# Performance work log

Hardware: AMD Instinct MI355X
Metric: run time of the kernel (lower is better)

The kernel has to match this reference:

```python
import jax, jax.numpy as jnp
import numpy as np

NUM_LAYERS = 2


def _lstm_scan(x, w_ih, w_hh):
    """x: [S,B,I]; w_ih: [4H,I]; w_hh: [4H,H]. Returns per-step (hs, cs): [S,B,H]."""
    S, B, _ = x.shape
    H = w_hh.shape[1]
    xg = jnp.einsum('sbi,gi->sbg', x, w_ih)  # precompute input contributions [S,B,4H]

    def step(carry, xg_t):
        h, c = carry
        gates = xg_t + h @ w_hh.T
        i, f, g, o = jnp.split(gates, 4, axis=-1)  # torch LSTM gate order
        i = jax.nn.sigmoid(i)
        f = jax.nn.sigmoid(f)
        g = jnp.tanh(g)
        o = jax.nn.sigmoid(o)
        c = f * c + i * g
        h = o * jnp.tanh(c)
        return (h, c), (h, c)

    init = (jnp.zeros((B, H), x.dtype), jnp.zeros((B, H), x.dtype))
    _, (hs, cs) = jax.lax.scan(step, init, xg)
    return hs, cs


def _stacked(x, w_ih, w_hh, reverse):
    """Stacked unidirectional LSTM. w_ih/w_hh: [L,4H,*].
    Returns (out [S,B,H], h_last [L,B,H], c_last [L,B,H]) matching stackedRNN
    semantics: for reverse, the returned 'last' hidden is the per-step state at
    original time index S-1 (first step processed in the reverse loop)."""
    h_last, c_last = [], []
    cur = x
    for layer in range(w_ih.shape[0]):
        xin = jnp.flip(cur, axis=0) if reverse else cur
        hs, cs = _lstm_scan(xin, w_ih[layer], w_hh[layer])
        if reverse:
            hs = jnp.flip(hs, axis=0)
            cs = jnp.flip(cs, axis=0)
        cur = hs
        h_last.append(hs[-1])  # faithful to torch code's layer[-1] indexing
        c_last.append(cs[-1])
    return cur, jnp.stack(h_last, 0), jnp.stack(c_last, 0)


def setup_inputs() -> dict:
    key = jax.random.key(0)
    ks = jax.random.split(key, 5)
    S, B, I, H, L = 256, 32, 1024, 1024, NUM_LAYERS
    stdev = 1.0 / np.sqrt(H)
    u = lambda k, shape: jax.random.uniform(k, shape, jnp.float32, -stdev, stdev)
    return {
        'x': jax.random.normal(ks[0], (S, B, I), jnp.float32),
        'w_ih_fwd': u(ks[1], (L, 4 * H, I)),
        'w_hh_fwd': u(ks[2], (L, 4 * H, H)),
        'w_ih_bwd': u(ks[3], (L, 4 * H, I)),
        'w_hh_bwd': u(ks[4], (L, 4 * H, H)),
    }


def reference(x, w_ih_fwd, w_hh_fwd, w_ih_bwd, w_hh_bwd):
    out_f, h_f, c_f = _stacked(x, w_ih_fwd, w_hh_fwd, reverse=False)
    out_b, h_b, c_b = _stacked(x, w_ih_bwd, w_hh_bwd, reverse=True)
    output = jnp.concatenate([out_f, out_b], axis=-1)      # [S,B,2H]
    h_all = jnp.concatenate([h_f, h_b], axis=-1)            # [L,B,2H]
    c_all = jnp.concatenate([c_f, c_b], axis=-1)            # [L,B,2H]
    return output, h_all, c_all
```

## Files before the change

kernel.cpp:

```cpp
#include <hip/hip_runtime.h>
#include <stdint.h>

#define SEQ   256
#define BSZ   32
#define HD    1024
#define GD    4096
#define KD    1024
#define MROWS (SEQ*BSZ)
#define PBLK  128
#define PTHR  512

typedef unsigned short u16;
typedef __attribute__((ext_vector_type(8))) __bf16 bf8_t;
typedef __attribute__((ext_vector_type(4))) float  f4_t;
typedef __attribute__((ext_vector_type(4))) unsigned int u4_t;

__device__ __forceinline__ u16 f2bf(float f) {
  unsigned u = __float_as_uint(f);
  u += 0x7fffu + ((u >> 16) & 1u);
  return (u16)(u >> 16);
}
__device__ __forceinline__ float bf2f(u16 s) {
  return __uint_as_float(((unsigned)s) << 16);
}
__device__ __forceinline__ void async_copy16(const void* g, void* l) {
  __builtin_amdgcn_global_load_lds(
      (const __attribute__((address_space(1))) void*)g,
      (__attribute__((address_space(3))) void*)l, 16, 0, 0);
}
__device__ __forceinline__ float sigm(float x) { return 1.0f / (1.0f + __expf(-x)); }
__device__ __forceinline__ float tanh_f(float x) {
  float e = __expf(-2.0f * x);
  return 2.0f / (1.0f + e) - 1.0f;
}

__global__ void cvt_f32_bf16(const float* __restrict__ src, u16* __restrict__ dst, int n4) {
  int i = blockIdx.x * blockDim.x + threadIdx.x;
  if (i >= n4) return;
  float4 v = ((const float4*)src)[i];
  ushort4 o;
  o.x = f2bf(v.x); o.y = f2bf(v.y); o.z = f2bf(v.z); o.w = f2bf(v.w);
  ((ushort4*)dst)[i] = o;
}

__global__ void reorder_whh(const float* __restrict__ src, u16* __restrict__ dst, int d) {
  int r = blockIdx.x;
  int layer = r >> 12, row = r & 4095;
  int g = row >> 10, j = row & 1023;
  int jblk = j >> 4, jl = j & 15;
  size_t drow = ((size_t)(d * 2 + layer) * 64 + jblk) * 64 + g * 16 + jl;
  float4 v = ((const float4*)(src + (size_t)r * KD))[threadIdx.x];
  ushort4 o;
  o.x = f2bf(v.x); o.y = f2bf(v.y); o.z = f2bf(v.z); o.w = f2bf(v.w);
  ((ushort4*)(dst + drow * KD))[threadIdx.x] = o;
}

__global__ __launch_bounds__(256) void gemm_bt(
    const u16* __restrict__ A, const u16* __restrict__ B, u16* __restrict__ C,
    int M, int N, int K)
{
  __shared__ u16 lA[128 * 32];
  __shared__ u16 lB[128 * 32];
  const int tid  = threadIdx.x;
  const int wave = tid >> 6, lane = tid & 63;
  const int wr = (wave >> 1) * 64, wc = (wave & 1) * 64;
  const int m0 = blockIdx.x * 128, n0 = blockIdx.y * 128;

  f4_t acc[4][4] = {};

  const int r0 = tid >> 2,          kp0 = (tid & 3) * 8;
  const int r1 = (tid + 256) >> 2,  kp1 = (tid & 3) * 8;
  const u16* gA0 = A + (size_t)(m0 + r0) * K + kp0;
  const u16* gA1 = A + (size_t)(m0 + r1) * K + kp1;
  const u16* gB0 = B + (size_t)(n0 + r0) * K + kp0;
  const u16* gB1 = B + (size_t)(n0 + r1) * K + kp1;
  u16* lA0 = lA + wave * 512;          u16* lA1 = lA + 2048 + wave * 512;
  u16* lB0 = lB + wave * 512;          u16* lB1 = lB + 2048 + wave * 512;

  const int fr = lane & 15, fk = (lane >> 4) * 8;

  for (int k0 = 0; k0 < K; k0 += 32) {
    async_copy16(gA0 + k0, lA0);
    async_copy16(gA1 + k0, lA1);
    async_copy16(gB0 + k0, lB0);
    async_copy16(gB1 + k0, lB1);
    __syncthreads();
    bf8_t af[4], bf[4];
    #pragma unroll
    for (int i = 0; i < 4; i++) af[i] = *(const bf8_t*)&lA[(wr + i * 16 + fr) * 32 + fk];
    #pragma unroll
    for (int i = 0; i < 4; i++) bf[i] = *(const bf8_t*)&lB[(wc + i * 16 + fr) * 32 + fk];
    #pragma unroll
    for (int mi = 0; mi < 4; mi++)
      #pragma unroll
      for (int ni = 0; ni < 4; ni++)
        acc[mi][ni] = __builtin_amdgcn_mfma_f32_16x16x32_bf16(af[mi], bf[ni], acc[mi][ni], 0, 0, 0);
    __syncthreads();
  }
  const int er = (lane >> 4) * 4, ec = lane & 15;
  #pragma unroll
  for (int mi = 0; mi < 4; mi++)
    #pragma unroll
    for (int ni = 0; ni < 4; ni++)
      #pragma unroll
      for (int r = 0; r < 4; r++) {
        int m = m0 + wr + mi * 16 + er + r;
        int n = n0 + wc + ni * 16 + ec;
        C[(size_t)m * N + n] = f2bf(acc[mi][ni][r]);
      }
}

__global__ __launch_bounds__(PTHR) void lstm_persist(
    const u16* __restrict__ whh_r,
    const u16* __restrict__ xg,
    u16*       __restrict__ htraj,
    float*     __restrict__ dout,
    unsigned*  __restrict__ cntb,
    int layer)
{
  const int tid = threadIdx.x;
  const int lane = tid & 63;
  const int mt = (tid >> 6) >> 1, kh = (tid >> 6) & 1;
  const int d = blockIdx.x & 1, jblk = blockIdx.x >> 1;
  const int j0 = jblk * 16;
  const int fr = lane & 15, quad = lane >> 4;
  unsigned* cnt = cntb + (size_t)d * 512;

  __builtin_amdgcn_fence(__ATOMIC_ACQUIRE, "agent");

  __shared__ __align__(16) uint32_t lH[32 * 512];
  float* lAcc = (float*)lH;

  u4_t wreg[16];
  {
    const u16* wp = whh_r
        + ((size_t)(((d * 2 + layer) * 64 + jblk) * 64 + mt * 16 + fr)) * KD
        + kh * 512 + quad * 8;
    #pragma unroll
    for (int ks = 0; ks < 16; ks++) wreg[ks] = *(const u4_t*)(wp + ks * 32);
    #pragma unroll
    for (int ks = 0; ks < 16; ks++) asm volatile("" : "+v"(wreg[ks]));
  }

  const int b_ = tid >> 3, jp = tid & 7;
  float cr0 = 0.0f, cr1 = 0.0f;

  uint32_t xv[4] = {};
  if (tid < 256) {
    const int tt0 = d ? (SEQ - 1) : 0;
    const uint32_t* xgp = (const uint32_t*)(xg
        + ((size_t)d * MROWS + (size_t)tt0 * BSZ + b_) * GD + j0) + jp;
    #pragma unroll
    for (int g = 0; g < 4; g++) xv[g] = xgp[g * 512];
  }

  for (int t = 0; t < SEQ; t++) {
    const int tt = d ? (SEQ - 1 - t) : t;

    if (t > 0) {
      const int ttp = d ? (tt + 1) : (tt - 1);
      const unsigned long long* hs8 = (const unsigned long long*)(htraj
          + ((size_t)d * MROWS + (size_t)ttp * BSZ) * HD);
      unsigned long long hv2[16];
      #pragma unroll
      for (int g = 0; g < 8; g++) {
        size_t c = (size_t)(g * 512 + tid) * 2;
        hv2[2 * g]     = __hip_atomic_load(hs8 + c,     __ATOMIC_RELAXED, __HIP_MEMORY_SCOPE_AGENT);
        hv2[2 * g + 1] = __hip_atomic_load(hs8 + c + 1, __ATOMIC_RELAXED, __HIP_MEMORY_SCOPE_AGENT);
      }
      #pragma unroll
      for (int g = 0; g < 8; g++) {
        int lc = g * 512 + tid;
        int row = lc >> 7, c = lc & 127;
        int pc = c ^ (row & 7);
        uint2 lo = __builtin_bit_cast(uint2, hv2[2 * g]);
        uint2 hi = __builtin_bit_cast(uint2, hv2[2 * g + 1]);
        u4_t v; v.x = lo.x; v.y = lo.y; v.z = hi.x; v.w = hi.y;
        *(u4_t*)&lH[row * 512 + pc * 4] = v;
      }
      __syncthreads();

      f4_t acc0 = {}, acc1 = {};
      #pragma unroll
      for (int ks = 0; ks < 16; ks++) {
        int cbase = ((kh * 64 + ks * 4 + quad) ^ (fr & 7)) << 2;
        bf8_t a0 = *(const bf8_t*)&lH[fr * 512 + cbase];
        bf8_t a1 = *(const bf8_t*)&lH[(fr + 16) * 512 + cbase];
        bf8_t wb = __builtin_bit_cast(bf8_t, wreg[ks]);
        acc0 = __builtin_amdgcn_mfma_f32_16x16x32_bf16(a0, wb, acc0, 0, 0, 0);
        acc1 = __builtin_amdgcn_mfma_f32_16x16x32_bf16(a1, wb, acc1, 0, 0, 0);
      }
      __syncthreads();

      #pragma unroll
      for (int r = 0; r < 4; r++) {
        lAcc[((mt * 2 + kh) * 32 + quad * 4 + r) * 16 + fr]      = acc0[r];
        lAcc[((mt * 2 + kh) * 32 + 16 + quad * 4 + r) * 16 + fr] = acc1[r];
      }
      __syncthreads();
    }

    if (tid < 256) {
      float vg0[4], vg1[4];
      #pragma unroll
      for (int g = 0; g < 4; g++) {
        float s0 = 0.f, s1 = 0.f;
        if (t > 0) {
          float2 p0 = *(const float2*)&lAcc[((g * 2 + 0) * 32 + b_) * 16 + 2 * jp];
          float2 p1 = *(const float2*)&lAcc[((g * 2 + 1) * 32 + b_) * 16 + 2 * jp];
          s0 = p0.x + p1.x; s1 = p0.y + p1.y;
        }
        vg0[g] = s0 + bf2f((u16)(xv[g] & 0xffffu));
        vg1[g] = s1 + bf2f((u16)(xv[g] >> 16));
      }
      float i0 = sigm(vg0[0]), f0 = sigm(vg0[1]), g0 = tanh_f(vg0[2]), o0 = sigm(vg0[3]);
      float i1 = sigm(vg1[0]), f1 = sigm(vg1[1]), g1 = tanh_f(vg1[2]), o1 = sigm(vg1[3]);
      cr0 = f0 * cr0 + i0 * g0;
      cr1 = f1 * cr1 + i1 * g1;
      float hn0 = o0 * tanh_f(cr0), hn1 = o1 * tanh_f(cr1);
      uint32_t hnp = ((uint32_t)f2bf(hn1) << 16) | (uint32_t)f2bf(hn0);

      size_t hq = (((size_t)d * MROWS + (size_t)tt * BSZ + b_) * HD + j0 + 2 * jp) >> 1;
      __hip_atomic_store((uint32_t*)htraj + hq, hnp, __ATOMIC_RELAXED, __HIP_MEMORY_SCOPE_AGENT);

      if (layer == 1) {
        float2 o2 = make_float2(hn0, hn1);
        *(float2*)&dout[((size_t)tt * BSZ + b_) * (2 * HD) + (size_t)d * HD + j0 + 2 * jp] = o2;
      }
      if ((d == 0 && t == SEQ - 1) || (d == 1 && t == 0)) {
        size_t hoff = (size_t)MROWS * 2 * HD + ((size_t)layer * BSZ + b_) * (2 * HD)
                    + (size_t)d * HD + j0 + 2 * jp;
        dout[hoff] = hn0;  dout[hoff + 1] = hn1;
        dout[hoff + (size_t)2 * BSZ * 2 * HD]     = cr0;
        dout[hoff + (size_t)2 * BSZ * 2 * HD + 1] = cr1;
      }
    }

    asm volatile("s_waitcnt vmcnt(0)" ::: "memory");
    uint32_t xvn[4] = {};
    if (t + 1 < SEQ && tid < 256) {
      const int ttn = d ? (SEQ - 2 - t) : (t + 1);
      const uint32_t* xgp = (const uint32_t*)(xg
          + ((size_t)d * MROWS + (size_t)ttn * BSZ + b_) * GD + j0) + jp;
      #pragma unroll
      for (int g = 0; g < 4; g++) xvn[g] = xgp[g * 512];
    }

    __syncthreads();
    if (tid == 0) {
      const unsigned sub = (unsigned)((blockIdx.x >> 1) & 7);
      unsigned old = __hip_atomic_fetch_add(&cnt[16 * (1 + sub)], 1u,
                                            __ATOMIC_RELAXED, __HIP_MEMORY_SCOPE_AGENT);
      if (old + 1u == 8u * (unsigned)(t + 1))
        __hip_atomic_fetch_add(&cnt[0], 1u, __ATOMIC_RELAXED, __HIP_MEMORY_SCOPE_AGENT);
      const unsigned goal = 8u * (unsigned)(t + 1);
      long spins = 0;
      while (__hip_atomic_load(&cnt[0], __ATOMIC_RELAXED, __HIP_MEMORY_SCOPE_AGENT) < goal) {
        if (++spins > (1L << 27)) break;
      }
    }
    __syncthreads();
    asm volatile("" ::: "memory");
    #pragma unroll
    for (int g = 0; g < 4; g++) xv[g] = xvn[g];
  }
}

extern "C" void kernel_launch(void* const* d_in, const int* in_sizes, int n_in,
                              void* d_out, int out_size, void* d_ws, size_t ws_size,
                              hipStream_t stream) {
  const float* x    = (const float*)d_in[0];
  const float* wihf = (const float*)d_in[1];
  const float* whhf = (const float*)d_in[2];
  const float* wihb = (const float*)d_in[3];
  const float* whhb = (const float*)d_in[4];
  float* out = (float*)d_out;

  const size_t NE = (size_t)MROWS * KD;
  char* ws = (char*)d_ws;
  u16*   xbf  = (u16*)ws;
  u16*   wih  = (u16*)(ws + NE * 2);
  u16*   whhr = wih + 2 * NE;
  u16*   xg   = whhr + 2 * NE;
  u16*   h0   = xg + (size_t)2 * MROWS * GD;
  unsigned* cnt = (unsigned*)(h0 + (size_t)2 * MROWS * HD);

  const int n4 = (int)(NE / 4);
  const int cg = n4 / 256;
  cvt_f32_bf16<<<cg, 256, 0, stream>>>(x,    xbf,      n4);
  cvt_f32_bf16<<<cg, 256, 0, stream>>>(wihf, wih,      n4);
  cvt_f32_bf16<<<cg, 256, 0, stream>>>(wihb, wih + NE, n4);
  reorder_whh<<<2 * GD, 256, 0, stream>>>(whhf, whhr, 0);
  reorder_whh<<<2 * GD, 256, 0, stream>>>(whhb, whhr, 1);

  hipMemsetAsync(cnt, 0, 4 * 512 * sizeof(unsigned), stream);

  dim3 gg(MROWS / 128, GD / 128);

  for (int d = 0; d < 2; d++)
    gemm_bt<<<gg, 256, 0, stream>>>(xbf, wih + (size_t)(d * 2) * GD * KD,
                                    xg + (size_t)d * MROWS * GD, MROWS, GD, KD);
  lstm_persist<<<PBLK, PTHR, 0, stream>>>(whhr, xg, h0, out, cnt, 0);

  for (int d = 0; d < 2; d++)
    gemm_bt<<<gg, 256, 0, stream>>>(h0 + (size_t)d * MROWS * HD,
                                    wih + (size_t)(d * 2 + 1) * GD * KD,
                                    xg + (size_t)d * MROWS * GD, MROWS, GD, KD);
  lstm_persist<<<PBLK, PTHR, 0, stream>>>(whhr, xg, h0, out, cnt + 1024, 1);
}
```

Before: 3.266 ms.

## Replace global counter barrier with per-block flags and targeted consumer waits

```diff
diff --git a/kernel.cpp b/kernel.cpp
--- a/kernel.cpp
+++ b/kernel.cpp
@@ -115,21 +115,22 @@
     const u16* __restrict__ xg,
     u16*       __restrict__ htraj,
     float*     __restrict__ dout,
-    unsigned*  __restrict__ cntb,
+    unsigned*  __restrict__ flagsb,
     int layer)
 {
   const int tid = threadIdx.x;
   const int lane = tid & 63;
-  const int mt = (tid >> 6) >> 1, kh = (tid >> 6) & 1;
+  const int wv  = tid >> 6;
+  const int mt = wv >> 1, kh = wv & 1;
   const int d = blockIdx.x & 1, jblk = blockIdx.x >> 1;
   const int j0 = jblk * 16;
   const int fr = lane & 15, quad = lane >> 4;
-  unsigned* cnt = cntb + (size_t)d * 512;
+  unsigned* flags = flagsb + (size_t)d * 512;
 
   __builtin_amdgcn_fence(__ATOMIC_ACQUIRE, "agent");
 
   __shared__ __align__(16) uint32_t lH[32 * 512];
-  float* lAcc = (float*)lH;
+  __shared__ __align__(16) float lAcc[4096];
 
   u4_t wreg[16];
   {
@@ -158,25 +159,45 @@
     const int tt = d ? (SEQ - 1 - t) : t;
 
     if (t > 0) {
-      const int ttp = d ? (tt + 1) : (tt - 1);
-      const unsigned long long* hs8 = (const unsigned long long*)(htraj
-          + ((size_t)d * MROWS + (size_t)ttp * BSZ) * HD);
-      unsigned long long hv2[16];
-      #pragma unroll
-      for (int g = 0; g < 8; g++) {
-        size_t c = (size_t)(g * 512 + tid) * 2;
-        hv2[2 * g]     = __hip_atomic_load(hs8 + c,     __ATOMIC_RELAXED, __HIP_MEMORY_SCOPE_AGENT);
-        hv2[2 * g + 1] = __hip_atomic_load(hs8 + c + 1, __ATOMIC_RELAXED, __HIP_MEMORY_SCOPE_AGENT);
-      }
-      #pragma unroll
-      for (int g = 0; g < 8; g++) {
-        int lc = g * 512 + tid;
-        int row = lc >> 7, c = lc & 127;
-        int pc = c ^ (row & 7);
-        uint2 lo = __builtin_bit_cast(uint2, hv2[2 * g]);
-        uint2 hi = __builtin_bit_cast(uint2, hv2[2 * g + 1]);
-        u4_t v; v.x = lo.x; v.y = lo.y; v.z = hi.x; v.w = hi.y;
-        *(u4_t*)&lH[row * 512 + pc * 4] = v;
+      if (wv >= 4) {
+        const int q = wv - 4;
+        {
+          long spins = 0;
+          for (;;) {
+            unsigned v = __hip_atomic_load(&flags[q * 64 + lane],
+                __ATOMIC_RELAXED, __HIP_MEMORY_SCOPE_AGENT);
+            if (__all((int)(v >= (unsigned)t))) break;
+            if (++spins > (1L << 24)) break;
+          }
+        }
+        asm volatile("" ::: "memory");
+        const int ttp = d ? (tt + 1) : (tt - 1);
+        const unsigned long long* hs8 = (const unsigned long long*)(htraj
+            + ((size_t)d * MROWS + (size_t)ttp * BSZ) * HD);
+        #pragma unroll
+        for (int hf = 0; hf < 2; hf++) {
+          unsigned long long hv2[16];
+          #pragma unroll
+          for (int k = 0; k < 8; k++) {
+            int kk  = hf * 8 + k;
+            int row = q * 8 + (kk >> 1);
+            int c   = (kk & 1) * 64 + lane;
+            size_t ci = ((size_t)row * 128 + c) * 2;
+            hv2[2 * k]     = __hip_atomic_load(hs8 + ci,     __ATOMIC_RELAXED, __HIP_MEMORY_SCOPE_AGENT);
+            hv2[2 * k + 1] = __hip_atomic_load(hs8 + ci + 1, __ATOMIC_RELAXED, __HIP_MEMORY_SCOPE_AGENT);
+          }
+          #pragma unroll
+          for (int k = 0; k < 8; k++) {
+            int kk  = hf * 8 + k;
+            int row = q * 8 + (kk >> 1);
+            int c   = (kk & 1) * 64 + lane;
+            int pc  = c ^ (row & 7);
+            uint2 lo = __builtin_bit_cast(uint2, hv2[2 * k]);
+            uint2 hi = __builtin_bit_cast(uint2, hv2[2 * k + 1]);
+            u4_t v; v.x = lo.x; v.y = lo.y; v.z = hi.x; v.w = hi.y;
+            *(u4_t*)&lH[row * 512 + pc * 4] = v;
+          }
+        }
       }
       __syncthreads();
 
@@ -190,15 +211,13 @@
         acc0 = __builtin_amdgcn_mfma_f32_16x16x32_bf16(a0, wb, acc0, 0, 0, 0);
         acc1 = __builtin_amdgcn_mfma_f32_16x16x32_bf16(a1, wb, acc1, 0, 0, 0);
       }
-      __syncthreads();
-
       #pragma unroll
       for (int r = 0; r < 4; r++) {
         lAcc[((mt * 2 + kh) * 32 + quad * 4 + r) * 16 + fr]      = acc0[r];
         lAcc[((mt * 2 + kh) * 32 + 16 + quad * 4 + r) * 16 + fr] = acc1[r];
       }
-      __syncthreads();
     }
+    __syncthreads();
 
     if (tid < 256) {
       float vg0[4], vg1[4];
@@ -234,35 +253,20 @@
         dout[hoff + (size_t)2 * BSZ * 2 * HD]     = cr0;
         dout[hoff + (size_t)2 * BSZ * 2 * HD + 1] = cr1;
       }
+
+      asm volatile("s_waitcnt vmcnt(0)" ::: "memory");
+      if (lane == 0)
+        __hip_atomic_store(&flags[wv * 64 + jblk], (unsigned)(t + 1),
+                           __ATOMIC_RELAXED, __HIP_MEMORY_SCOPE_AGENT);
+
+      if (t + 1 < SEQ) {
+        const int ttn = d ? (SEQ - 2 - t) : (t + 1);
+        const uint32_t* xgp = (const uint32_t*)(xg
+            + ((size_t)d * MROWS + (size_t)ttn * BSZ + b_) * GD + j0) + jp;
+        #pragma unroll
+        for (int g = 0; g < 4; g++) xv[g] = xgp[g * 512];
+      }
     }
-
-    asm volatile("s_waitcnt vmcnt(0)" ::: "memory");
-    uint32_t xvn[4] = {};
-    if (t + 1 < SEQ && tid < 256) {
-      const int ttn = d ? (SEQ - 2 - t) : (t + 1);
-      const uint32_t* xgp = (const uint32_t*)(xg
-          + ((size_t)d * MROWS + (size_t)ttn * BSZ + b_) * GD + j0) + jp;
-      #pragma unroll
-      for (int g = 0; g < 4; g++) xvn[g] = xgp[g * 512];
-    }
-
-    __syncthreads();
-    if (tid == 0) {
-      const unsigned sub = (unsigned)((blockIdx.x >> 1) & 7);
-      unsigned old = __hip_atomic_fetch_add(&cnt[16 * (1 + sub)], 1u,
-                                            __ATOMIC_RELAXED, __HIP_MEMORY_SCOPE_AGENT);
-      if (old + 1u == 8u * (unsigned)(t + 1))
-        __hip_atomic_fetch_add(&cnt[0], 1u, __ATOMIC_RELAXED, __HIP_MEMORY_SCOPE_AGENT);
-      const unsigned goal = 8u * (unsigned)(t + 1);
-      long spins = 0;
-      while (__hip_atomic_load(&cnt[0], __ATOMIC_RELAXED, __HIP_MEMORY_SCOPE_AGENT) < goal) {
-        if (++spins > (1L << 27)) break;
-      }
-    }
-    __syncthreads();
-    asm volatile("" ::: "memory");
-    #pragma unroll
-    for (int g = 0; g < 4; g++) xv[g] = xvn[g];
   }
 }
 
```

After: 3.722 ms. 1.14x slower.
